# Kernel optimization log

Measured on AMD Instinct MI355X. Metric: run time of the kernel, lower is better.

## Reference

```python
import jax, jax.numpy as jnp
import numpy as np

DISTANCE_W = 1.0
ANGLE_W = 1.0
EPS = 1e-12  # matches F.normalize eps


def setup_inputs() -> dict:
    key = jax.random.key(0)
    k1, k2 = jax.random.split(key)
    student_emb = jax.random.normal(k1, (1024, 512), dtype=jnp.float32)
    teacher_emb = jax.random.normal(k2, (1024, 512), dtype=jnp.float32)
    return {"student_emb": student_emb, "teacher_emb": teacher_emb}


def _pairwise_similarity(emb):
    # F.normalize(emb, dim=1) then emb @ emb.T -> [N, N] cosine similarity
    norm = jnp.maximum(jnp.linalg.norm(emb, axis=1, keepdims=True), EPS)
    en = emb / norm
    return en @ en.T


def _angle_similarity(emb):
    # ||e_i - e_j||^2 for all pairs, computed via the GEMM expansion
    # (same math as the N x N x D broadcast in the original, no O(N^2 D) tensor)
    sq = jnp.sum(emb * emb, axis=1)  # [N]
    gram = emb @ emb.T               # [N, N]
    return sq[:, None] + sq[None, :] - 2.0 * gram


def reference(student_emb, teacher_emb):
    loss_dist = jnp.mean((_pairwise_similarity(student_emb) - _pairwise_similarity(teacher_emb)) ** 2)
    loss_angle = jnp.mean((_angle_similarity(student_emb) - _angle_similarity(teacher_emb)) ** 2)
    return DISTANCE_W * loss_dist + ANGLE_W * loss_angle
```

## Files before the change

kernel.cpp:

```cpp
#include <hip/hip_runtime.h>

typedef short short8 __attribute__((ext_vector_type(8)));
typedef float f32x16 __attribute__((ext_vector_type(16)));
typedef unsigned short ushort;
typedef unsigned long long u64;

#define DD 512
#define NBLK 272
#define MAGIC 0x9E3779B97F4A7C15ULL


__device__ __forceinline__ short to_bf16(float f) {
    unsigned int u = __float_as_uint(f);
    u += 0x7FFFu + ((u >> 16) & 1u);
    return (short)(u >> 16);
}

__device__ __forceinline__ short8 pack8(float4 a, float4 b) {
    short8 r;
    r[0] = to_bf16(a.x); r[1] = to_bf16(a.y); r[2] = to_bf16(a.z); r[3] = to_bf16(a.w);
    r[4] = to_bf16(b.x); r[5] = to_bf16(b.y); r[6] = to_bf16(b.z); r[7] = to_bf16(b.w);
    return r;
}

__device__ __forceinline__ float dot4(float4 v) {
    return v.x*v.x + v.y*v.y + v.z*v.z + v.w*v.w;
}

__global__ __launch_bounds__(128) void rkd_fused(const float* __restrict__ S,
                                                 const float* __restrict__ T,
                                                 ushort* __restrict__ bf,
                                                 float* __restrict__ sqarr,
                                                 u64* __restrict__ conv_tag,
                                                 u64* __restrict__ done_tag,
                                                 float* __restrict__ done_val,
                                                 float* __restrict__ out) {
    __shared__ ushort tiles[2][12288];
    __shared__ float statI[4][32];
    __shared__ float statJ[4][64];
    __shared__ float wsum[2];

    const int t   = threadIdx.x;
    const int blk = blockIdx.x;

    if (blk < 256) {
        const int rl  = t >> 4;
        const int l16 = t & 15;
        const int r   = (blk << 3) + rl;
        const float* src = (r < 1024) ? (S + (size_t)r * DD)
                                      : (T + (size_t)(r - 1024) * DD);
        ushort* dst = bf + (size_t)r * DD;
        float s = 0.0f;
        #pragma unroll
        for (int j = 0; j < 4; ++j) {
            const int chunk = l16 + 16 * j;
            float4 v0 = ((const float4*)src)[chunk * 2];
            float4 v1 = ((const float4*)src)[chunk * 2 + 1];
            *(short8*)(dst + chunk * 8) = pack8(v0, v1);
            s += dot4(v0) + dot4(v1);
        }
        #pragma unroll
        for (int off = 8; off > 0; off >>= 1) s += __shfl_down(s, off, 16);
        if (l16 == 0) {
            sqarr[r]        = s;
            sqarr[2048 + r] = 1.0f / fmaxf(sqrtf(s), 1e-12f);
        }
        __syncthreads();
        if (t == 0) {
            __threadfence();
            __hip_atomic_store(&conv_tag[blk], MAGIC,
                               __ATOMIC_RELAXED, __HIP_MEMORY_SCOPE_AGENT);
        }
    }

    int rem = blk, a = 0;
    for (;;) { int cnt = 16 - (a >> 1); if (rem < cnt) break; rem -= cnt; ++a; }
    const int b2 = (a >> 1) + rem;
    const int I = a * 32;
    const int J = b2 * 64;

    if (t < 24) {
        int idx;
        if      (t < 4)  idx = (I >> 3) + t;
        else if (t < 8)  idx = 128 + (I >> 3) + (t - 4);
        else if (t < 16) idx = (J >> 3) + (t - 8);
        else             idx = 128 + (J >> 3) + (t - 16);
        while (__hip_atomic_load(&conv_tag[idx], __ATOMIC_RELAXED,
                                 __HIP_MEMORY_SCOPE_AGENT) != MAGIC)
            __builtin_amdgcn_s_sleep(2);
    }
    __syncthreads();
    __threadfence();

    const int w = t >> 6;
    const int L = t & 63;
    const int c = L & 31;
    const int h = L >> 5;
    const int colsel = w * 32;

    const ushort* bS = bf;
    const ushort* bT = bf + (size_t)1024 * DD;

    {
        const int a2 = t >> 5, r = t & 31;
        statI[a2][r]      = sqarr[a2 * 1024 + I + r];
        statJ[a2][r]      = sqarr[a2 * 1024 + J + r];
        statJ[a2][32 + r] = sqarr[a2 * 1024 + J + 32 + r];
    }

    const int lrow  = L >> 3;
    const int lchk  = (L & 7) ^ lrow;
    const int lgoff = lrow * DD + lchk * 8;

    const ushort* gtab[12];
    int loff[12];
    #pragma unroll
    for (int j = 0; j < 12; ++j) {
        const int q = w * 12 + j;
        const ushort* gmat; int gbase, lo, sub;
        if (q < 4)       { gmat = bS; gbase = I; sub = q;      lo = 0    + sub * 512; }
        else if (q < 8)  { gmat = bT; gbase = I; sub = q - 4;  lo = 2048 + sub * 512; }
        else if (q < 16) { gmat = bS; gbase = J; sub = q - 8;  lo = 4096 + sub * 512; }
        else             { gmat = bT; gbase = J; sub = q - 16; lo = 8192 + sub * 512; }
        gtab[j] = gmat + (size_t)(gbase + sub * 8) * DD + lgoff;
        loff[j] = lo;
    }

    f32x16 accS, accT;
    #pragma unroll
    for (int i2 = 0; i2 < 16; ++i2) { accS[i2] = 0.0f; accT[i2] = 0.0f; }

    #pragma unroll
    for (int j = 0; j < 12; ++j)
        __builtin_amdgcn_global_load_lds(
            (const __attribute__((address_space(1))) void*)(gtab[j]),
            (__attribute__((address_space(3))) void*)(&tiles[0][0] + loff[j]), 16, 0, 0);

    for (int i = 0; i < 8; ++i) {
        __syncthreads();
        if (i < 7) {
            const int k0 = (i + 1) * 64;
            ushort* nb = &tiles[(i + 1) & 1][0];
            #pragma unroll
            for (int j = 0; j < 12; ++j)
                __builtin_amdgcn_global_load_lds(
                    (const __attribute__((address_space(1))) void*)(gtab[j] + k0),
                    (__attribute__((address_space(3))) void*)(nb + loff[j]), 16, 0, 0);
        }
        const ushort* base = &tiles[i & 1][0];
        #pragma unroll
        for (int step = 0; step < 4; ++step) {
            const int us = ((step * 2 + h) ^ (c & 7)) * 8;
            short8 afS = *(const short8*)(base + c * 64 + us);
            short8 afT = *(const short8*)(base + 2048 + c * 64 + us);
            short8 bS8 = *(const short8*)(base + 4096 + (colsel + c) * 64 + us);
            short8 bT8 = *(const short8*)(base + 8192 + (colsel + c) * 64 + us);
            accS = __builtin_amdgcn_mfma_f32_32x32x16_bf16(afS, bS8, accS, 0, 0, 0);
            accT = __builtin_amdgcn_mfma_f32_32x32x16_bf16(afT, bT8, accT, 0, 0, 0);
        }
    }

    const int colg = colsel + c;
    const int jg   = J + colg;
    const float js  = statJ[0][colg], jt  = statJ[1][colg];
    const float rjs = statJ[2][colg], rjt = statJ[3][colg];

    float local = 0.0f;
    #pragma unroll
    for (int reg = 0; reg < 16; ++reg) {
        const int rowg = (reg & 3) + 8 * (reg >> 2) + 4 * h;
        const int ig = I + rowg;
        float wgt = (jg > ig) ? 2.0f : ((jg == ig) ? 1.0f : 0.0f);
        float is  = statI[0][rowg], it  = statI[1][rowg];
        float ris = statI[2][rowg], rit = statI[3][rowg];
        float gs = accS[reg], gt = accT[reg];
        float d1 = gs * ris * rjs - gt * rit * rjt;
        float d2 = (is + js - 2.0f * gs) - (it + jt - 2.0f * gt);
        local += wgt * (d1 * d1 + d2 * d2);
    }

    #pragma unroll
    for (int off = 32; off > 0; off >>= 1) local += __shfl_down(local, off);
    if (L == 0) wsum[w] = local;
    __syncthreads();

    if (t == 0) {
        done_val[blk] = wsum[0] + wsum[1];
        __threadfence();
        __hip_atomic_store(&done_tag[blk], MAGIC,
                           __ATOMIC_RELAXED, __HIP_MEMORY_SCOPE_AGENT);
    }

    if (blk == 0) {
        for (int i = t; i < NBLK; i += 128)
            while (__hip_atomic_load(&done_tag[i], __ATOMIC_RELAXED,
                                     __HIP_MEMORY_SCOPE_AGENT) != MAGIC)
                __builtin_amdgcn_s_sleep(2);
        __syncthreads();
        __threadfence();
        float part = 0.0f;
        for (int i = t; i < NBLK; i += 128) part += done_val[i];
        #pragma unroll
        for (int off = 32; off > 0; off >>= 1) part += __shfl_down(part, off);
        if ((t & 63) == 0) wsum[t >> 6] = part;
        __syncthreads();
        if (t == 0) out[0] = (wsum[0] + wsum[1]) * (1.0f / 1048576.0f);
    }
}

extern "C" void kernel_launch(void* const* d_in, const int* in_sizes, int n_in,
                              void* d_out, int out_size, void* d_ws, size_t ws_size,
                              hipStream_t stream) {
    const float* S = (const float*)d_in[0];
    const float* T = (const float*)d_in[1];
    char* ws = (char*)d_ws;
    ushort* bf      = (ushort*)ws;
    float*  sqarr   = (float*)(ws + 2 * 1024 * 1024);
    u64*    conv_tag = (u64*)(ws + 2 * 1024 * 1024 + 16384);
    u64*    done_tag = (u64*)(ws + 2 * 1024 * 1024 + 16384 + 2048);
    float*  done_val = (float*)(ws + 2 * 1024 * 1024 + 16384 + 2048 + 2176);

    rkd_fused<<<NBLK, 128, 0, stream>>>(S, T, bf, sqarr, conv_tag, done_tag, done_val,
                                        (float*)d_out);
}
```

Baseline: 86.84 us.

## Fuse bf16 conversion and row norms into GEMM tile loads, drop prepass phase

Removes the separate conversion phase that wrote bf16 copies and squared norms to a workspace, along with the inter-block spin-wait on conversion tags. Each block now loads fp32 tiles of S and T directly into registers, computes squared-norm partials while packing to bf16 into swizzled LDS, and reduces the norms in-block after the K loop. Global loads for the next K step are register-prefetched instead of using async global_load_lds, and the final reduction moves to the last block. The cost is that every block rereads and reconverts fp32 rows, which doubles global read bytes per tile, uses more registers, and adds an extra barrier per K step.

```diff
diff --git a/kernel.cpp b/kernel.cpp
--- a/kernel.cpp
+++ b/kernel.cpp
@@ -27,14 +27,11 @@
     return v.x*v.x + v.y*v.y + v.z*v.z + v.w*v.w;
 }
 
-__global__ __launch_bounds__(128) void rkd_fused(const float* __restrict__ S,
-                                                 const float* __restrict__ T,
-                                                 ushort* __restrict__ bf,
-                                                 float* __restrict__ sqarr,
-                                                 u64* __restrict__ conv_tag,
-                                                 u64* __restrict__ done_tag,
-                                                 float* __restrict__ done_val,
-                                                 float* __restrict__ out) {
+__global__ __launch_bounds__(128) void rkd_one(const float* __restrict__ S,
+                                               const float* __restrict__ T,
+                                               u64* __restrict__ done_tag,
+                                               float* __restrict__ done_val,
+                                               float* __restrict__ out) {
     __shared__ ushort tiles[2][12288];
     __shared__ float statI[4][32];
     __shared__ float statJ[4][64];
@@ -43,109 +40,64 @@
     const int t   = threadIdx.x;
     const int blk = blockIdx.x;
 
-    if (blk < 256) {
-        const int rl  = t >> 4;
-        const int l16 = t & 15;
-        const int r   = (blk << 3) + rl;
-        const float* src = (r < 1024) ? (S + (size_t)r * DD)
-                                      : (T + (size_t)(r - 1024) * DD);
-        ushort* dst = bf + (size_t)r * DD;
-        float s = 0.0f;
-        #pragma unroll
-        for (int j = 0; j < 4; ++j) {
-            const int chunk = l16 + 16 * j;
-            float4 v0 = ((const float4*)src)[chunk * 2];
-            float4 v1 = ((const float4*)src)[chunk * 2 + 1];
-            *(short8*)(dst + chunk * 8) = pack8(v0, v1);
-            s += dot4(v0) + dot4(v1);
-        }
-        #pragma unroll
-        for (int off = 8; off > 0; off >>= 1) s += __shfl_down(s, off, 16);
-        if (l16 == 0) {
-            sqarr[r]        = s;
-            sqarr[2048 + r] = 1.0f / fmaxf(sqrtf(s), 1e-12f);
-        }
-        __syncthreads();
-        if (t == 0) {
-            __threadfence();
-            __hip_atomic_store(&conv_tag[blk], MAGIC,
-                               __ATOMIC_RELAXED, __HIP_MEMORY_SCOPE_AGENT);
-        }
-    }
-
     int rem = blk, a = 0;
     for (;;) { int cnt = 16 - (a >> 1); if (rem < cnt) break; rem -= cnt; ++a; }
     const int b2 = (a >> 1) + rem;
     const int I = a * 32;
     const int J = b2 * 64;
 
-    if (t < 24) {
-        int idx;
-        if      (t < 4)  idx = (I >> 3) + t;
-        else if (t < 8)  idx = 128 + (I >> 3) + (t - 4);
-        else if (t < 16) idx = (J >> 3) + (t - 8);
-        else             idx = 128 + (J >> 3) + (t - 16);
-        while (__hip_atomic_load(&conv_tag[idx], __ATOMIC_RELAXED,
-                                 __HIP_MEMORY_SCOPE_AGENT) != MAGIC)
-            __builtin_amdgcn_s_sleep(2);
-    }
-    __syncthreads();
-    __threadfence();
-
     const int w = t >> 6;
     const int L = t & 63;
     const int c = L & 31;
     const int h = L >> 5;
     const int colsel = w * 32;
+    const int lrow   = L >> 3;
+    const int c8     = (L & 7) ^ lrow;
 
-    const ushort* bS = bf;
-    const ushort* bT = bf + (size_t)1024 * DD;
-
-    {
-        const int a2 = t >> 5, r = t & 31;
-        statI[a2][r]      = sqarr[a2 * 1024 + I + r];
-        statJ[a2][r]      = sqarr[a2 * 1024 + J + r];
-        statJ[a2][32 + r] = sqarr[a2 * 1024 + J + 32 + r];
-    }
-
-    const int lrow  = L >> 3;
-    const int lchk  = (L & 7) ^ lrow;
-    const int lgoff = lrow * DD + lchk * 8;
-
-    const ushort* gtab[12];
-    int loff[12];
+    const float* gsrc[12];
+    int ldst[12];
     #pragma unroll
     for (int j = 0; j < 12; ++j) {
         const int q = w * 12 + j;
-        const ushort* gmat; int gbase, lo, sub;
-        if (q < 4)       { gmat = bS; gbase = I; sub = q;      lo = 0    + sub * 512; }
-        else if (q < 8)  { gmat = bT; gbase = I; sub = q - 4;  lo = 2048 + sub * 512; }
-        else if (q < 16) { gmat = bS; gbase = J; sub = q - 8;  lo = 4096 + sub * 512; }
-        else             { gmat = bT; gbase = J; sub = q - 16; lo = 8192 + sub * 512; }
-        gtab[j] = gmat + (size_t)(gbase + sub * 8) * DD + lgoff;
-        loff[j] = lo;
+        const float* gm; int gbase, lo, sub;
+        if (q < 4)       { gm = S; gbase = I; sub = q;      lo = 0;    }
+        else if (q < 8)  { gm = T; gbase = I; sub = q - 4;  lo = 2048; }
+        else if (q < 16) { gm = S; gbase = J; sub = q - 8;  lo = 4096; }
+        else             { gm = T; gbase = J; sub = q - 16; lo = 8192; }
+        gsrc[j] = gm + (size_t)(gbase + sub * 8 + lrow) * DD + c8 * 8;
+        ldst[j] = lo + sub * 512 + L * 8;
     }
+
+    float4 rv[12][2];
+    float  sqp[12];
+    #pragma unroll
+    for (int j = 0; j < 12; ++j) sqp[j] = 0.0f;
 
     f32x16 accS, accT;
     #pragma unroll
     for (int i2 = 0; i2 < 16; ++i2) { accS[i2] = 0.0f; accT[i2] = 0.0f; }
 
     #pragma unroll
-    for (int j = 0; j < 12; ++j)
-        __builtin_amdgcn_global_load_lds(
-            (const __attribute__((address_space(1))) void*)(gtab[j]),
-            (__attribute__((address_space(3))) void*)(&tiles[0][0] + loff[j]), 16, 0, 0);
+    for (int j = 0; j < 12; ++j) {
+        rv[j][0] = ((const float4*)gsrc[j])[0];
+        rv[j][1] = ((const float4*)gsrc[j])[1];
+    }
 
     for (int i = 0; i < 8; ++i) {
         __syncthreads();
+        ushort* db = &tiles[i & 1][0];
+        #pragma unroll
+        for (int j = 0; j < 12; ++j) {
+            sqp[j] += dot4(rv[j][0]) + dot4(rv[j][1]);
+            *(short8*)(db + ldst[j]) = pack8(rv[j][0], rv[j][1]);
+        }
+        __syncthreads();
         if (i < 7) {
-            const int k0 = (i + 1) * 64;
-            ushort* nb = &tiles[(i + 1) & 1][0];
             #pragma unroll
-            for (int j = 0; j < 12; ++j)
-                __builtin_amdgcn_global_load_lds(
-                    (const __attribute__((address_space(1))) void*)(gtab[j] + k0),
-                    (__attribute__((address_space(3))) void*)(nb + loff[j]), 16, 0, 0);
+            for (int j = 0; j < 12; ++j) {
+                rv[j][0] = ((const float4*)(gsrc[j] + (i + 1) * 64))[0];
+                rv[j][1] = ((const float4*)(gsrc[j] + (i + 1) * 64))[1];
+            }
         }
         const ushort* base = &tiles[i & 1][0];
         #pragma unroll
@@ -159,6 +111,23 @@
             accT = __builtin_amdgcn_mfma_f32_32x32x16_bf16(afT, bT8, accT, 0, 0, 0);
         }
     }
+
+    #pragma unroll
+    for (int j = 0; j < 12; ++j) {
+        float s = sqp[j];
+        s += __shfl_xor(s, 1);
+        s += __shfl_xor(s, 2);
+        s += __shfl_xor(s, 4);
+        if ((L & 7) == 0) {
+            const float rn = 1.0f / fmaxf(sqrtf(s), 1e-12f);
+            const int q = w * 12 + j;
+            if (q < 4)       { statI[0][q*8        + lrow] = s; statI[2][q*8        + lrow] = rn; }
+            else if (q < 8)  { statI[1][(q-4)*8    + lrow] = s; statI[3][(q-4)*8    + lrow] = rn; }
+            else if (q < 16) { statJ[0][(q-8)*8    + lrow] = s; statJ[2][(q-8)*8    + lrow] = rn; }
+            else             { statJ[1][(q-16)*8   + lrow] = s; statJ[3][(q-16)*8   + lrow] = rn; }
+        }
+    }
+    __syncthreads();
 
     const int colg = colsel + c;
     const int jg   = J + colg;
@@ -191,15 +160,15 @@
                            __ATOMIC_RELAXED, __HIP_MEMORY_SCOPE_AGENT);
     }
 
-    if (blk == 0) {
-        for (int i = t; i < NBLK; i += 128)
-            while (__hip_atomic_load(&done_tag[i], __ATOMIC_RELAXED,
+    if (blk == NBLK - 1) {
+        for (int i2 = t; i2 < NBLK; i2 += 128)
+            while (__hip_atomic_load(&done_tag[i2], __ATOMIC_RELAXED,
                                      __HIP_MEMORY_SCOPE_AGENT) != MAGIC)
                 __builtin_amdgcn_s_sleep(2);
         __syncthreads();
         __threadfence();
         float part = 0.0f;
-        for (int i = t; i < NBLK; i += 128) part += done_val[i];
+        for (int i2 = t; i2 < NBLK; i2 += 128) part += done_val[i2];
         #pragma unroll
         for (int off = 32; off > 0; off >>= 1) part += __shfl_down(part, off);
         if ((t & 63) == 0) wsum[t >> 6] = part;
@@ -214,12 +183,8 @@
     const float* S = (const float*)d_in[0];
     const float* T = (const float*)d_in[1];
     char* ws = (char*)d_ws;
-    ushort* bf      = (ushort*)ws;
-    float*  sqarr   = (float*)(ws + 2 * 1024 * 1024);
-    u64*    conv_tag = (u64*)(ws + 2 * 1024 * 1024 + 16384);
-    u64*    done_tag = (u64*)(ws + 2 * 1024 * 1024 + 16384 + 2048);
-    float*  done_val = (float*)(ws + 2 * 1024 * 1024 + 16384 + 2048 + 2176);
+    u64*   done_tag = (u64*)ws;
+    float* done_val = (float*)(ws + 4096);
 
-    rkd_fused<<<NBLK, 128, 0, stream>>>(S, T, bf, sqarr, conv_tag, done_tag, done_val,
-                                        (float*)d_out);
+    rkd_one<<<NBLK, 128, 0, stream>>>(S, T, done_tag, done_val, (float*)d_out);
 }
```

After: 83.38 us. 4.0% less time.
